# Kernel tuning notes

Hardware: AMD Instinct MI355X
Metric: run time of the kernel (lower is better)

The kernel has to match this reference:

```python
import jax, jax.numpy as jnp
import numpy as np

K = 16
BN_EPS = 1e-5


def setup_inputs() -> dict:
    key = jax.random.key(0)
    ks = jax.random.split(key, 6)
    B, N, D, P = 16, 1024, 1024, 256
    return {
        "points": jax.random.normal(ks[0], (B, N, 3), jnp.float32),
        "features": jax.random.normal(ks[1], (B, N, D), jnp.float32),
        "W_down": jax.random.normal(ks[2], (D, P), jnp.float32) * (1.0 / np.sqrt(D)),
        "b_down": jnp.zeros((P,), jnp.float32),
        "W_edge": jax.random.normal(ks[3], (2 * P, P), jnp.float32) * (1.0 / np.sqrt(2 * P)),
        "b_edge": jnp.zeros((P,), jnp.float32),
        "bn_gamma": jnp.ones((P,), jnp.float32),
        "bn_beta": jnp.zeros((P,), jnp.float32),
        "bn_mean": jnp.zeros((P,), jnp.float32),
        "bn_var": jnp.ones((P,), jnp.float32),
        "W_up": jax.random.normal(ks[4], (P, D), jnp.float32) * (1.0 / np.sqrt(P)),
        "b_up": jnp.zeros((D,), jnp.float32),
    }


def reference(points, features, W_down, b_down, W_edge, b_edge,
              bn_gamma, bn_beta, bn_mean, bn_var, W_up, b_up):
    # proj_down + ReLU: (B, N, P)
    feats_low = jax.nn.relu(jnp.einsum("bnd,dp->bnp", features, W_down) + b_down)

    # pairwise squared distances via the |a|^2 + |b|^2 - 2 a.b identity (B, N, N)
    sq = jnp.sum(points * points, axis=-1)
    d2 = sq[:, :, None] + sq[:, None, :] - 2.0 * jnp.einsum("bnc,bmc->bnm", points, points)

    # k nearest neighbors (smallest distance) -> indices (B, N, K)
    _, idx = jax.lax.top_k(-d2, K)

    # gather neighbor features per batch: (B, N, K, P)
    neighbor_feats = jax.vmap(lambda f, i: f[i])(feats_low, idx)
    center_feats = feats_low[:, :, None, :]  # broadcast over K

    # edge features: [center, neighbor - center] -> (B, N, K, 2P)
    edge = jnp.concatenate(
        [jnp.broadcast_to(center_feats, neighbor_feats.shape),
         neighbor_feats - center_feats], axis=-1)

    # edge_conv: Linear -> BatchNorm1d(eval, running stats) -> ReLU
    h = jnp.einsum("bnke,ep->bnkp", edge, W_edge) + b_edge
    h = (h - bn_mean) * jax.lax.rsqrt(bn_var + BN_EPS) * bn_gamma + bn_beta
    h = jax.nn.relu(h)

    # max aggregation over K neighbors -> (B, N, P)
    local = jnp.max(h, axis=2)

    # proj_up + residual
    return features + jnp.einsum("bnp,pd->bnd", local, W_up) + b_up
```

## Files before the change

kernel.cpp:

```cpp
#include <hip/hip_runtime.h>
#include <hip/hip_bf16.h>
#include <math.h>

#define BB 16
#define NN 1024
#define DD 1024
#define PP 256
#define KK 16
#define MROWS (BB*NN)

typedef short bf16x8 __attribute__((ext_vector_type(8)));
typedef float f32x4  __attribute__((ext_vector_type(4)));

__device__ __forceinline__ void async_copy16(const void* g, void* l) {
    __builtin_amdgcn_global_load_lds(
        (const __attribute__((address_space(1))) void*)g,
        (__attribute__((address_space(3))) void*)l, 16, 0, 0);
}

__global__ __launch_bounds__(256) void convert_bf16_kernel(
    const float* __restrict__ in, __hip_bfloat16* __restrict__ out)
{
    int i = blockIdx.x * 256 + threadIdx.x;
    float4 v = reinterpret_cast<const float4*>(in)[i];
    __hip_bfloat16 h0 = __float2bfloat16(v.x), h1 = __float2bfloat16(v.y);
    __hip_bfloat16 h2 = __float2bfloat16(v.z), h3 = __float2bfloat16(v.w);
    ushort4 o;
    o.x = *reinterpret_cast<unsigned short*>(&h0);
    o.y = *reinterpret_cast<unsigned short*>(&h1);
    o.z = *reinterpret_cast<unsigned short*>(&h2);
    o.w = *reinterpret_cast<unsigned short*>(&h3);
    reinterpret_cast<ushort4*>(out)[i] = o;
}

__global__ __launch_bounds__(256) void prep_wdt_kernel(
    const float* __restrict__ Wd, __hip_bfloat16* __restrict__ Wdt)
{
    int i = blockIdx.x * 256 + threadIdx.x;
    int p = i >> 10, d = i & 1023;
    Wdt[i] = __float2bfloat16(Wd[d * 256 + p]);
}

__global__ __launch_bounds__(256) void prep_wct_kernel(
    const float* __restrict__ We, __hip_bfloat16* __restrict__ Wct)
{
    int i = blockIdx.x * 256 + threadIdx.x;
    int n = i >> 8, d = i & 255;
    float v;
    if (n < 256) v = We[d * 256 + n] - We[(256 + d) * 256 + n];
    else         v = We[(256 + d) * 256 + (n - 256)];
    Wct[i] = __float2bfloat16(v);
}

__global__ __launch_bounds__(256) void prep_wut_kernel(
    const float* __restrict__ Wu, __hip_bfloat16* __restrict__ Wut)
{
    int i = blockIdx.x * 256 + threadIdx.x;
    int dd = i >> 8, p = i & 255;
    Wut[i] = __float2bfloat16(Wu[p * 1024 + dd]);
}

template<bool RELU, bool BIAS, bool ADDSRC, bool OUTBF16>
__global__ __launch_bounds__(256) void gemm_mfma_kernel(
    const __hip_bfloat16* __restrict__ A,
    const __hip_bfloat16* __restrict__ Bt,
    const float* __restrict__ bias,
    const float* __restrict__ src,
    void* __restrict__ Cout,
    int M, int N, int K)
{
    __shared__ __align__(16) __hip_bfloat16 As[128 * 32];
    __shared__ __align__(16) __hip_bfloat16 Bs[128 * 32];

    const int tid  = threadIdx.x;
    const int lane = tid & 63;
    const int wave = tid >> 6;
    const int wr = wave >> 1, wc = wave & 1;
    const int row0 = blockIdx.y * 128;
    const int col0 = blockIdx.x * 128;

    const int g  = lane >> 4;
    const int lr = lane & 15;

    const int srow = (lane >> 2);
    const int scol = (lane & 3) * 8;

    f32x4 acc[4][4];
    #pragma unroll
    for (int m = 0; m < 4; ++m)
        #pragma unroll
        for (int n = 0; n < 4; ++n)
            acc[m][n] = (f32x4){0.f, 0.f, 0.f, 0.f};

    for (int k0 = 0; k0 < K; k0 += 32) {
        __syncthreads();
        #pragma unroll
        for (int r = 0; r < 2; ++r) {
            const int c = r * 4 + wave;
            const int arow = c * 16 + srow;
            async_copy16(A  + (row0 + arow) * (long)K + k0 + scol, As + c * 512);
            async_copy16(Bt + (col0 + arow) * (long)K + k0 + scol, Bs + c * 512);
        }
        __syncthreads();

        bf16x8 af[4], bfr[4];
        #pragma unroll
        for (int m = 0; m < 4; ++m)
            af[m] = *reinterpret_cast<const bf16x8*>(
                &As[(wr * 64 + m * 16 + lr) * 32 + g * 8]);
        #pragma unroll
        for (int n = 0; n < 4; ++n)
            bfr[n] = *reinterpret_cast<const bf16x8*>(
                &Bs[(wc * 64 + n * 16 + lr) * 32 + g * 8]);
        #pragma unroll
        for (int m = 0; m < 4; ++m)
            #pragma unroll
            for (int n = 0; n < 4; ++n)
                acc[m][n] = __builtin_amdgcn_mfma_f32_16x16x32_bf16(
                    af[m], bfr[n], acc[m][n], 0, 0, 0);
    }

    const int orow = row0 + wr * 64;
    const int ocol = col0 + wc * 64;
    #pragma unroll
    for (int m = 0; m < 4; ++m) {
        #pragma unroll
        for (int n = 0; n < 4; ++n) {
            const int gc = ocol + n * 16 + lr;
            const float bv = BIAS ? bias[gc] : 0.f;
            #pragma unroll
            for (int j = 0; j < 4; ++j) {
                const int gr = orow + m * 16 + g * 4 + j;
                float v = acc[m][n][j] + bv;
                if (ADDSRC) v += src[(long)gr * N + gc];
                if (RELU)   v = fmaxf(v, 0.f);
                if (OUTBF16)
                    reinterpret_cast<__hip_bfloat16*>(Cout)[(long)gr * N + gc] =
                        __float2bfloat16(v);
                else
                    reinterpret_cast<float*>(Cout)[(long)gr * N + gc] = v;
            }
        }
    }
}

__global__ __launch_bounds__(256) void knn_kernel(
    const float* __restrict__ points, int* __restrict__ idx_out)
{
    __shared__ float px[NN], py[NN], pz[NN], psq[NN];
    const int b = blockIdx.x;
    const int tid = threadIdx.x;
    const float* P = points + (long)b * NN * 3;
    for (int i = tid; i < NN; i += 256) {
        float x = P[i * 3 + 0], y = P[i * 3 + 1], z = P[i * 3 + 2];
        px[i] = x; py[i] = y; pz[i] = z;
        psq[i] = x * x + y * y + z * z;
    }
    __syncthreads();

    const int wave = tid >> 6, lane = tid & 63;
    const int n = blockIdx.y * 4 + wave;
    const float xn = px[n], yn = py[n], zn = pz[n], sqn = psq[n];

    float d[16];
    #pragma unroll
    for (int j = 0; j < 16; ++j) {
        int m = lane + 64 * j;
        float dot = xn * px[m] + yn * py[m] + zn * pz[m];
        d[j] = (sqn + psq[m]) - 2.0f * dot;
    }

    int* out = idx_out + ((long)b * NN + n) * KK;
    for (int it = 0; it < KK; ++it) {
        float bv = d[0]; int bj = 0;
        #pragma unroll
        for (int j = 1; j < 16; ++j)
            if (d[j] < bv) { bv = d[j]; bj = j; }
        int bm = lane + 64 * bj;
        #pragma unroll
        for (int off = 1; off < 64; off <<= 1) {
            float ov = __shfl_xor(bv, off);
            int   om = __shfl_xor(bm, off);
            if (ov < bv || (ov == bv && om < bm)) { bv = ov; bm = om; }
        }
        if ((bm & 63) == lane) d[bm >> 6] = 3.0e38f;
        if (lane == 0) out[it] = bm;
    }
}

__global__ __launch_bounds__(256) void edge_max_kernel(
    const __hip_bfloat16* __restrict__ cn,
    const int*   __restrict__ idx,
    const float* __restrict__ b_edge,
    const float* __restrict__ gamma, const float* __restrict__ beta,
    const float* __restrict__ mean,  const float* __restrict__ var,
    __hip_bfloat16* __restrict__ local)
{
    const long row = blockIdx.x;
    const int  p   = threadIdx.x;
    const long bbase = (row >> 10) << 10;

    __shared__ int sidx[KK];
    if (p < KK) sidx[p] = idx[row * KK + p];
    __syncthreads();

    float mx = -3.0e38f, mn = 3.0e38f;
    #pragma unroll
    for (int k = 0; k < KK; ++k) {
        float v = __bfloat162float(cn[(bbase + sidx[k]) * 512 + 256 + p]);
        mx = fmaxf(mx, v);
        mn = fminf(mn, v);
    }
    float c = __bfloat162float(cn[row * 512 + p]);
    float s = gamma[p] * rsqrtf(var[p] + 1e-5f);
    float t = beta[p] - mean[p] * s;
    float nsel = (s >= 0.f) ? mx : mn;
    local[row * 256 + p] = __float2bfloat16(fmaxf(0.f, s * (c + b_edge[p] + nsel) + t));
}

extern "C" void kernel_launch(void* const* d_in, const int* in_sizes, int n_in,
                              void* d_out, int out_size, void* d_ws, size_t ws_size,
                              hipStream_t stream)
{
    const float* points   = (const float*)d_in[0];
    const float* features = (const float*)d_in[1];
    const float* W_down   = (const float*)d_in[2];
    const float* b_down   = (const float*)d_in[3];
    const float* W_edge   = (const float*)d_in[4];
    const float* b_edge   = (const float*)d_in[5];
    const float* bn_gamma = (const float*)d_in[6];
    const float* bn_beta  = (const float*)d_in[7];
    const float* bn_mean  = (const float*)d_in[8];
    const float* bn_var   = (const float*)d_in[9];
    const float* W_up     = (const float*)d_in[10];
    const float* b_up     = (const float*)d_in[11];
    float* out = (float*)d_out;

    char* w = (char*)d_ws;
    __hip_bfloat16* featuresh = (__hip_bfloat16*)w;
    __hip_bfloat16* cn        = (__hip_bfloat16*)w;
    __hip_bfloat16* local     = (__hip_bfloat16*)(w + (16ul << 20));
    __hip_bfloat16* feats_low = (__hip_bfloat16*)(w + (32ul << 20));
    char* wtail = w + (40ul << 20);
    __hip_bfloat16* Wdt = (__hip_bfloat16*)wtail;
    __hip_bfloat16* Wct = (__hip_bfloat16*)(wtail + 524288);
    __hip_bfloat16* Wut = (__hip_bfloat16*)(wtail + 524288 + 262144);
    int* nidx = (int*)(wtail + 524288 + 262144 + 524288);

    convert_bf16_kernel<<<MROWS * DD / 4 / 256, 256, 0, stream>>>(features, featuresh);
    prep_wdt_kernel<<<1024, 256, 0, stream>>>(W_down, Wdt);
    prep_wct_kernel<<<512, 256, 0, stream>>>(W_edge, Wct);
    prep_wut_kernel<<<1024, 256, 0, stream>>>(W_up, Wut);
    knn_kernel<<<dim3(BB, NN / 4), 256, 0, stream>>>(points, nidx);

    gemm_mfma_kernel<true, true, false, true><<<dim3(2, 128), 256, 0, stream>>>(
        featuresh, Wdt, b_down, nullptr, feats_low, MROWS, 256, 1024);

    gemm_mfma_kernel<false, false, false, true><<<dim3(4, 128), 256, 0, stream>>>(
        feats_low, Wct, nullptr, nullptr, cn, MROWS, 512, 256);

    edge_max_kernel<<<MROWS, 256, 0, stream>>>(
        cn, nidx, b_edge, bn_gamma, bn_beta, bn_mean, bn_var, local);

    gemm_mfma_kernel<false, true, true, false><<<dim3(8, 128), 256, 0, stream>>>(
        local, Wut, b_up, features, out, MROWS, 1024, 256);
}
```

Before: 287.3 us.

## Fuse fp32-to-bf16 conversion into GEMM, merge weight prep, rewrite kNN and edge-max

Drops the standalone features-to-bf16 conversion pass. The first GEMM now loads fp32 A tiles through registers and converts them into LDS, which saves a full write and read of a 32 MB bf16 copy. The three weight-prep kernels become one launch. kNN now handles two queries per wave using packed (distance, index) doubles, a register bitonic sort and a 32-lane merge, and edge_max processes 8 rows per block with 16-byte vector loads. The fp32 A path loses async global-to-LDS copies and is synchronous, and clamping distances at zero could change tie ordering.

```diff
diff --git a/kernel.cpp b/kernel.cpp
--- a/kernel.cpp
+++ b/kernel.cpp
@@ -11,6 +11,7 @@
 
 typedef short bf16x8 __attribute__((ext_vector_type(8)));
 typedef float f32x4  __attribute__((ext_vector_type(4)));
+typedef unsigned short u16x8 __attribute__((ext_vector_type(8)));
 
 __device__ __forceinline__ void async_copy16(const void* g, void* l) {
     __builtin_amdgcn_global_load_lds(
@@ -18,51 +19,33 @@
         (__attribute__((address_space(3))) void*)l, 16, 0, 0);
 }
 
-__global__ __launch_bounds__(256) void convert_bf16_kernel(
-    const float* __restrict__ in, __hip_bfloat16* __restrict__ out)
-{
-    int i = blockIdx.x * 256 + threadIdx.x;
-    float4 v = reinterpret_cast<const float4*>(in)[i];
-    __hip_bfloat16 h0 = __float2bfloat16(v.x), h1 = __float2bfloat16(v.y);
-    __hip_bfloat16 h2 = __float2bfloat16(v.z), h3 = __float2bfloat16(v.w);
-    ushort4 o;
-    o.x = *reinterpret_cast<unsigned short*>(&h0);
-    o.y = *reinterpret_cast<unsigned short*>(&h1);
-    o.z = *reinterpret_cast<unsigned short*>(&h2);
-    o.w = *reinterpret_cast<unsigned short*>(&h3);
-    reinterpret_cast<ushort4*>(out)[i] = o;
-}
-
-__global__ __launch_bounds__(256) void prep_wdt_kernel(
-    const float* __restrict__ Wd, __hip_bfloat16* __restrict__ Wdt)
-{
-    int i = blockIdx.x * 256 + threadIdx.x;
-    int p = i >> 10, d = i & 1023;
-    Wdt[i] = __float2bfloat16(Wd[d * 256 + p]);
-}
-
-__global__ __launch_bounds__(256) void prep_wct_kernel(
-    const float* __restrict__ We, __hip_bfloat16* __restrict__ Wct)
-{
-    int i = blockIdx.x * 256 + threadIdx.x;
-    int n = i >> 8, d = i & 255;
-    float v;
-    if (n < 256) v = We[d * 256 + n] - We[(256 + d) * 256 + n];
-    else         v = We[(256 + d) * 256 + (n - 256)];
-    Wct[i] = __float2bfloat16(v);
-}
-
-__global__ __launch_bounds__(256) void prep_wut_kernel(
-    const float* __restrict__ Wu, __hip_bfloat16* __restrict__ Wut)
-{
-    int i = blockIdx.x * 256 + threadIdx.x;
-    int dd = i >> 8, p = i & 255;
-    Wut[i] = __float2bfloat16(Wu[p * 1024 + dd]);
-}
-
-template<bool RELU, bool BIAS, bool ADDSRC, bool OUTBF16>
+__global__ __launch_bounds__(256) void prep_weights_kernel(
+    const float* __restrict__ Wd, const float* __restrict__ We,
+    const float* __restrict__ Wu,
+    __hip_bfloat16* __restrict__ Wdt, __hip_bfloat16* __restrict__ Wct,
+    __hip_bfloat16* __restrict__ Wut)
+{
+    int blk = blockIdx.x;
+    if (blk < 1024) {
+        int i = blk * 256 + threadIdx.x;
+        int p = i >> 10, d = i & 1023;
+        Wdt[i] = __float2bfloat16(Wd[d * 256 + p]);
+    } else if (blk < 1536) {
+        int i = (blk - 1024) * 256 + threadIdx.x;
+        int n = i >> 8, d = i & 255;
+        float v = (n < 256) ? (We[d * 256 + n] - We[(256 + d) * 256 + n])
+                            : We[(256 + d) * 256 + (n - 256)];
+        Wct[i] = __float2bfloat16(v);
+    } else {
+        int i = (blk - 1536) * 256 + threadIdx.x;
+        int dd = i >> 8, p = i & 255;
+        Wut[i] = __float2bfloat16(Wu[p * 1024 + dd]);
+    }
+}
+
+template<bool RELU, bool BIAS, bool ADDSRC, bool OUTBF16, bool AFP32>
 __global__ __launch_bounds__(256) void gemm_mfma_kernel(
-    const __hip_bfloat16* __restrict__ A,
+    const void* __restrict__ A,
     const __hip_bfloat16* __restrict__ Bt,
     const float* __restrict__ bias,
     const float* __restrict__ src,
@@ -71,6 +54,9 @@
 {
     __shared__ __align__(16) __hip_bfloat16 As[128 * 32];
     __shared__ __align__(16) __hip_bfloat16 Bs[128 * 32];
+
+    const __hip_bfloat16* Ah = (const __hip_bfloat16*)A;
+    const float*          Af = (const float*)A;
 
     const int tid  = threadIdx.x;
     const int lane = tid & 63;
@@ -93,20 +79,46 @@
             acc[m][n] = (f32x4){0.f, 0.f, 0.f, 0.f};
 
     for (int k0 = 0; k0 < K; k0 += 32) {
+        float4 av[4];
+        if (AFP32) {
+            #pragma unroll
+            for (int q = 0; q < 4; ++q) {
+                int li = q * 256 + tid;
+                av[q] = *reinterpret_cast<const float4*>(
+                    &Af[(long)(row0 + (li >> 3)) * K + k0 + (li & 7) * 4]);
+            }
+        }
         __syncthreads();
         #pragma unroll
         for (int r = 0; r < 2; ++r) {
             const int c = r * 4 + wave;
             const int arow = c * 16 + srow;
-            async_copy16(A  + (row0 + arow) * (long)K + k0 + scol, As + c * 512);
+            if (!AFP32)
+                async_copy16(Ah + (row0 + arow) * (long)K + k0 + scol, As + c * 512);
             async_copy16(Bt + (col0 + arow) * (long)K + k0 + scol, Bs + c * 512);
         }
+        if (AFP32) {
+            #pragma unroll
+            for (int q = 0; q < 4; ++q) {
+                int li = q * 256 + tid;
+                __hip_bfloat16 h0 = __float2bfloat16(av[q].x);
+                __hip_bfloat16 h1 = __float2bfloat16(av[q].y);
+                __hip_bfloat16 h2 = __float2bfloat16(av[q].z);
+                __hip_bfloat16 h3 = __float2bfloat16(av[q].w);
+                ushort4 o;
+                o.x = *reinterpret_cast<unsigned short*>(&h0);
+                o.y = *reinterpret_cast<unsigned short*>(&h1);
+                o.z = *reinterpret_cast<unsigned short*>(&h2);
+                o.w = *reinterpret_cast<unsigned short*>(&h3);
+                *reinterpret_cast<ushort4*>(&As[(li >> 3) * 32 + (li & 7) * 4]) = o;
+            }
+        }
         __syncthreads();
 
-        bf16x8 af[4], bfr[4];
+        bf16x8 afr[4], bfr[4];
         #pragma unroll
         for (int m = 0; m < 4; ++m)
-            af[m] = *reinterpret_cast<const bf16x8*>(
+            afr[m] = *reinterpret_cast<const bf16x8*>(
                 &As[(wr * 64 + m * 16 + lr) * 32 + g * 8]);
         #pragma unroll
         for (int n = 0; n < 4; ++n)
@@ -117,7 +129,7 @@
             #pragma unroll
             for (int n = 0; n < 4; ++n)
                 acc[m][n] = __builtin_amdgcn_mfma_f32_16x16x32_bf16(
-                    af[m], bfr[n], acc[m][n], 0, 0, 0);
+                    afr[m], bfr[n], acc[m][n], 0, 0, 0);
     }
 
     const int orow = row0 + wr * 64;
@@ -159,33 +171,66 @@
     __syncthreads();
 
     const int wave = tid >> 6, lane = tid & 63;
-    const int n = blockIdx.y * 4 + wave;
+    const int half = lane >> 5, r = lane & 31;
+    const int n = blockIdx.y * 8 + wave * 2 + half;
     const float xn = px[n], yn = py[n], zn = pz[n], sqn = psq[n];
 
-    float d[16];
-    #pragma unroll
-    for (int j = 0; j < 16; ++j) {
-        int m = lane + 64 * j;
+    double pk[32];
+    #pragma unroll
+    for (int j = 0; j < 32; ++j) {
+        int m = r + 32 * j;
         float dot = xn * px[m] + yn * py[m] + zn * pz[m];
-        d[j] = (sqn + psq[m]) - 2.0f * dot;
-    }
-
-    int* out = idx_out + ((long)b * NN + n) * KK;
-    for (int it = 0; it < KK; ++it) {
-        float bv = d[0]; int bj = 0;
-        #pragma unroll
-        for (int j = 1; j < 16; ++j)
-            if (d[j] < bv) { bv = d[j]; bj = j; }
-        int bm = lane + 64 * bj;
-        #pragma unroll
-        for (int off = 1; off < 64; off <<= 1) {
-            float ov = __shfl_xor(bv, off);
-            int   om = __shfl_xor(bm, off);
-            if (ov < bv || (ov == bv && om < bm)) { bv = ov; bm = om; }
-        }
-        if ((bm & 63) == lane) d[bm >> 6] = 3.0e38f;
-        if (lane == 0) out[it] = bm;
-    }
+        float d = (sqn + psq[m]) - 2.0f * dot;
+        d = fmaxf(d, 0.0f);
+        unsigned long long u =
+            ((unsigned long long)__float_as_uint(d) << 32) | (unsigned)m;
+        pk[j] = __longlong_as_double((long long)u);
+    }
+
+    #pragma unroll
+    for (int k = 2; k <= 32; k <<= 1) {
+        #pragma unroll
+        for (int j = k >> 1; j > 0; j >>= 1) {
+            #pragma unroll
+            for (int i = 0; i < 32; ++i) {
+                int ixj = i ^ j;
+                if (ixj > i) {
+                    double a = pk[i], c = pk[ixj];
+                    double lo_ = fmin(a, c), hi_ = fmax(a, c);
+                    if ((i & k) == 0) { pk[i] = lo_; pk[ixj] = hi_; }
+                    else              { pk[i] = hi_; pk[ixj] = lo_; }
+                }
+            }
+        }
+    }
+
+    double lm = pk[0];
+    int myidx = 0;
+    for (int it = 0; it < 16; ++it) {
+        unsigned hi = (unsigned)__double2hiint(lm);
+        unsigned lo = (unsigned)__double2loint(lm);
+        unsigned wh = hi;
+        #pragma unroll
+        for (int off = 1; off <= 16; off <<= 1) {
+            unsigned o = (unsigned)__shfl_xor((int)wh, off);
+            wh = (o < wh) ? o : wh;
+        }
+        unsigned lc = (hi == wh) ? lo : 0xFFFFFFFFu;
+        unsigned wl = lc;
+        #pragma unroll
+        for (int off = 1; off <= 16; off <<= 1) {
+            unsigned o = (unsigned)__shfl_xor((int)wl, off);
+            wl = (o < wl) ? o : wl;
+        }
+        if (r == it) myidx = (int)wl;
+        if ((hi == wh) && (lo == wl)) {
+            #pragma unroll
+            for (int j = 0; j < 16; ++j) pk[j] = pk[j + 1];
+            lm = pk[0];
+        }
+    }
+    if (r < 16)
+        idx_out[((long)b * NN + n) * KK + r] = myidx;
 }
 
 __global__ __launch_bounds__(256) void edge_max_kernel(
@@ -196,26 +241,49 @@
     const float* __restrict__ mean,  const float* __restrict__ var,
     __hip_bfloat16* __restrict__ local)
 {
-    const long row = blockIdx.x;
-    const int  p   = threadIdx.x;
+    const int tid  = threadIdx.x;
+    const int rsub = tid >> 5;
+    const int t    = tid & 31;
+    const long row = (long)blockIdx.x * 8 + rsub;
     const long bbase = (row >> 10) << 10;
-
-    __shared__ int sidx[KK];
-    if (p < KK) sidx[p] = idx[row * KK + p];
+    const int c0 = t * 8;
+
+    __shared__ int sidx[8][KK];
+    if (tid < 128)
+        sidx[tid >> 4][tid & 15] =
+            idx[((long)blockIdx.x * 8 + (tid >> 4)) * KK + (tid & 15)];
     __syncthreads();
 
-    float mx = -3.0e38f, mn = 3.0e38f;
+    float mx[8], mn[8];
+    #pragma unroll
+    for (int e = 0; e < 8; ++e) { mx[e] = -3.0e38f; mn[e] = 3.0e38f; }
+
     #pragma unroll
     for (int k = 0; k < KK; ++k) {
-        float v = __bfloat162float(cn[(bbase + sidx[k]) * 512 + 256 + p]);
-        mx = fmaxf(mx, v);
-        mn = fminf(mn, v);
-    }
-    float c = __bfloat162float(cn[row * 512 + p]);
-    float s = gamma[p] * rsqrtf(var[p] + 1e-5f);
-    float t = beta[p] - mean[p] * s;
-    float nsel = (s >= 0.f) ? mx : mn;
-    local[row * 256 + p] = __float2bfloat16(fmaxf(0.f, s * (c + b_edge[p] + nsel) + t));
+        u16x8 v = *reinterpret_cast<const u16x8*>(
+            cn + (bbase + sidx[rsub][k]) * 512 + 256 + c0);
+        #pragma unroll
+        for (int e = 0; e < 8; ++e) {
+            float f = __uint_as_float(((unsigned)v[e]) << 16);
+            mx[e] = fmaxf(mx[e], f);
+            mn[e] = fminf(mn[e], f);
+        }
+    }
+
+    u16x8 cv = *reinterpret_cast<const u16x8*>(cn + row * 512 + c0);
+    u16x8 o;
+    #pragma unroll
+    for (int e = 0; e < 8; ++e) {
+        const int c = c0 + e;
+        float s  = gamma[c] * rsqrtf(var[c] + 1e-5f);
+        float tt = beta[c] - mean[c] * s;
+        float cf = __uint_as_float(((unsigned)cv[e]) << 16);
+        float nsel = (s >= 0.f) ? mx[e] : mn[e];
+        float vr = fmaxf(0.f, s * (cf + b_edge[c] + nsel) + tt);
+        __hip_bfloat16 h = __float2bfloat16(vr);
+        o[e] = *reinterpret_cast<unsigned short*>(&h);
+    }
+    *reinterpret_cast<u16x8*>(local + row * 256 + c0) = o;
 }
 
 extern "C" void kernel_launch(void* const* d_in, const int* in_sizes, int n_in,
@@ -237,31 +305,27 @@
     float* out = (float*)d_out;
 
     char* w = (char*)d_ws;
-    __hip_bfloat16* featuresh = (__hip_bfloat16*)w;
     __hip_bfloat16* cn        = (__hip_bfloat16*)w;
     __hip_bfloat16* local     = (__hip_bfloat16*)(w + (16ul << 20));
-    __hip_bfloat16* feats_low = (__hip_bfloat16*)(w + (32ul << 20));
-    char* wtail = w + (40ul << 20);
+    __hip_bfloat16* feats_low = (__hip_bfloat16*)(w + (24ul << 20));
+    char* wtail = w + (32ul << 20);
     __hip_bfloat16* Wdt = (__hip_bfloat16*)wtail;
     __hip_bfloat16* Wct = (__hip_bfloat16*)(wtail + 524288);
     __hip_bfloat16* Wut = (__hip_bfloat16*)(wtail + 524288 + 262144);
     int* nidx = (int*)(wtail + 524288 + 262144 + 524288);
 
-    convert_bf16_kernel<<<MROWS * DD / 4 / 256, 256, 0, stream>>>(features, featuresh);
-    prep_wdt_kernel<<<1024, 256, 0, stream>>>(W_down, Wdt);
-    prep_wct_kernel<<<512, 256, 0, stream>>>(W_edge, Wct);
-    prep_wut_kernel<<<1024, 256, 0, stream>>>(W_up, Wut);
-    knn_kernel<<<dim3(BB, NN / 4), 256, 0, stream>>>(points, nidx);
-
-    gemm_mfma_kernel<true, true, false, true><<<dim3(2, 128), 256, 0, stream>>>(
-        featuresh, Wdt, b_down, nullptr, feats_low, MROWS, 256, 1024);
-
-    gemm_mfma_kernel<false, false, false, true><<<dim3(4, 128), 256, 0, stream>>>(
+    prep_weights_kernel<<<2560, 256, 0, stream>>>(W_down, W_edge, W_up, Wdt, Wct, Wut);
+    knn_kernel<<<dim3(BB, NN / 8), 256, 0, stream>>>(points, nidx);
+
+    gemm_mfma_kernel<true, true, false, true, true><<<dim3(2, 128), 256, 0, stream>>>(
+        features, Wdt, b_down, nullptr, feats_low, MROWS, 256, 1024);
+
+    gemm_mfma_kernel<false, false, false, true, false><<<dim3(4, 128), 256, 0, stream>>>(
         feats_low, Wct, nullptr, nullptr, cn, MROWS, 512, 256);
 
-    edge_max_kernel<<<MROWS, 256, 0, stream>>>(
+    edge_max_kernel<<<MROWS / 8, 256, 0, stream>>>(
         cn, nidx, b_edge, bn_gamma, bn_beta, bn_mean, bn_var, local);
 
-    gemm_mfma_kernel<false, true, true, false><<<dim3(8, 128), 256, 0, stream>>>(
+    gemm_mfma_kernel<false, true, true, false, false><<<dim3(8, 128), 256, 0, stream>>>(
         local, Wut, b_up, features, out, MROWS, 1024, 256);
 }
```

New measurement: 247.4 us. 1.16x faster.
